# Kernel optimization log

Measured on AMD Instinct MI355X. Metric: run time of the kernel, lower is better.

## Reference

```python
import jax, jax.numpy as jnp
import numpy as np

HIDDEN_DIM = 512
SCALE = HIDDEN_DIM ** (-0.5)


def setup_inputs() -> dict:
    key = jax.random.key(0)
    kx, kw = jax.random.split(key)
    x = jax.random.normal(kx, (4, 4096, HIDDEN_DIM), dtype=jnp.float32)
    # nn.Linear weight is [out, in]; y = x @ W.T. We store W in torch layout.
    Wq = jax.random.normal(kw, (HIDDEN_DIM, HIDDEN_DIM), dtype=jnp.float32) * (HIDDEN_DIM ** -0.5)
    return {"x": x, "Wq": Wq}


def reference(x, Wq):
    # Faithful to source: q, k, v all use the SAME q_matrix projection.
    q = jnp.einsum("bcd,ed->bce", x, Wq)  # [B, C, D]
    k = q
    v = q
    scores = jnp.einsum("bcd,bed->bce", q, k) * SCALE  # [B, C, C]
    attn = jax.nn.softmax(scores, axis=-1)
    # dropout p=0.0 -> identity
    y = jnp.einsum("bce,bed->bcd", attn, v)  # [B, C, D]
    return y
```

## Files before the change

### kernel.cpp

```cpp
#include <hip/hip_runtime.h>
#include <stdint.h>

typedef unsigned int u32;
typedef unsigned short u16;
typedef __attribute__((ext_vector_type(8))) short bf16x8;
typedef __attribute__((ext_vector_type(4))) float f32x4;

#define B_ 4
#define S_ 4096
#define D_ 512
#define SCALE_ 0.04419417382415922f

__device__ __forceinline__ u16 f2b(float f) {
  u32 u = __builtin_bit_cast(u32, f);
  return (u16)((u + 0x7FFFu + ((u >> 16) & 1u)) >> 16);
}
__device__ __forceinline__ float b2f(u16 h) {
  u32 u = ((u32)h) << 16;
  return __builtin_bit_cast(float, u);
}
__device__ __forceinline__ void gld16(const void* g, void* l) {
  __builtin_amdgcn_global_load_lds(
      (const __attribute__((address_space(1))) u32*)g,
      (__attribute__((address_space(3))) u32*)l, 16, 0, 0);
}

__global__ __launch_bounds__(256, 1) void qproj(
    const float* __restrict__ X, const float* __restrict__ W,
    u16* __restrict__ Qr, u16* __restrict__ Qt) {
  __shared__ __align__(16) u16 Wt[512 * 64];
  const int tid = threadIdx.x;
  const int wave = tid >> 6, lane = tid & 63;
  const int m16 = lane & 15, quad = lane >> 4;
  const int r0 = blockIdx.x * 64;

  f32x4 acc[32];
#pragma unroll
  for (int i = 0; i < 32; ++i) acc[i] = f32x4{};

  const float* xrow = X + (size_t)(r0 + wave * 16 + m16) * D_;

  for (int kc = 0; kc < 8; ++kc) {
#pragma unroll
    for (int rr = 0; rr < 2; ++rr) {
      int e = tid + rr * 256;
      const float* src = W + (size_t)e * D_ + kc * 64;
#pragma unroll
      for (int bl = 0; bl < 8; ++bl) {
        float4 a = ((const float4*)src)[bl * 2];
        float4 b = ((const float4*)src)[bl * 2 + 1];
        bf16x8 v;
        v[0] = (short)f2b(a.x); v[1] = (short)f2b(a.y);
        v[2] = (short)f2b(a.z); v[3] = (short)f2b(a.w);
        v[4] = (short)f2b(b.x); v[5] = (short)f2b(b.y);
        v[6] = (short)f2b(b.z); v[7] = (short)f2b(b.w);
        *(bf16x8*)(&Wt[e * 64 + ((bl + e) & 7) * 8]) = v;
      }
    }
    __syncthreads();
#pragma unroll
    for (int kk = 0; kk < 2; ++kk) {
      const float* ap = xrow + kc * 64 + kk * 32 + quad * 8;
      float4 a0 = ((const float4*)ap)[0];
      float4 a1 = ((const float4*)ap)[1];
      bf16x8 af;
      af[0] = (short)f2b(a0.x); af[1] = (short)f2b(a0.y);
      af[2] = (short)f2b(a0.z); af[3] = (short)f2b(a0.w);
      af[4] = (short)f2b(a1.x); af[5] = (short)f2b(a1.y);
      af[6] = (short)f2b(a1.z); af[7] = (short)f2b(a1.w);
      int jb = quad + 4 * kk;
#pragma unroll
      for (int nt = 0; nt < 32; ++nt) {
        int e = m16 + nt * 16;
        bf16x8 bf = *(const bf16x8*)(&Wt[e * 64 + ((jb + e) & 7) * 8]);
        acc[nt] = __builtin_amdgcn_mfma_f32_16x16x32_bf16(af, bf, acc[nt], 0, 0, 0);
      }
    }
    __syncthreads();
  }
  const int b = r0 >> 12;
  const int s0 = (r0 & (S_ - 1)) + wave * 16 + quad * 4;
  const int grow = r0 + wave * 16 + quad * 4;
#pragma unroll
  for (int nt = 0; nt < 32; ++nt) {
    int e = nt * 16 + m16;
    u16 h0 = f2b(acc[nt][0]), h1 = f2b(acc[nt][1]);
    u16 h2 = f2b(acc[nt][2]), h3 = f2b(acc[nt][3]);
    Qr[(size_t)(grow + 0) * D_ + e] = h0;
    Qr[(size_t)(grow + 1) * D_ + e] = h1;
    Qr[(size_t)(grow + 2) * D_ + e] = h2;
    Qr[(size_t)(grow + 3) * D_ + e] = h3;
    uint2 pv;
    pv.x = (u32)h0 | ((u32)h1 << 16);
    pv.y = (u32)h2 | ((u32)h3 << 16);
    *(uint2*)(&Qt[((size_t)(b * D_ + e)) * S_ + s0]) = pv;
  }
}

__global__ __launch_bounds__(256, 1) void flashattn(
    const u16* __restrict__ Qrow, const u16* __restrict__ Qt,
    float* __restrict__ Out) {
  __shared__ __align__(16) u16 Kt[64 * 512];
  __shared__ __align__(16) u16 Vt[512 * 64];
  __shared__ __align__(16) u16 Pl[4][16 * 88];

  const int tid = threadIdx.x;
  const int wave = tid >> 6, lane = tid & 63;
  const int m16 = lane & 15, quad = lane >> 4;
  const int qt = blockIdx.x, bb = blockIdx.y;
  const u16* Qb  = Qrow + (size_t)bb * S_ * D_;
  const u16* Qtb = Qt   + (size_t)bb * D_ * S_;

  bf16x8 qf[16];
  {
    const u16* qp = Qb + (size_t)(qt * 64 + wave * 16 + m16) * D_ + quad * 8;
#pragma unroll
    for (int ks = 0; ks < 16; ++ks) qf[ks] = *(const bf16x8*)(qp + ks * 32);
  }

  f32x4 o[32];
#pragma unroll
  for (int i = 0; i < 32; ++i) o[i] = f32x4{};
  float mrow[4] = {-1e30f, -1e30f, -1e30f, -1e30f};
  float lrow[4] = {0.f, 0.f, 0.f, 0.f};
  u16* pw = &Pl[wave][0];

  for (int kt = 0; kt < 64; ++kt) {
    {
      const u16* src = Qb + (size_t)(kt * 64) * D_;
#pragma unroll
      for (int t = 0; t < 16; ++t) {
        int n = wave * 16 + t;
        int gb = (lane & ~7) | ((lane + n) & 7);
        gld16(src + (size_t)n * D_ + gb * 8, &Kt[n * 512]);
      }
      const u16* vsrc = Qtb + kt * 64;
#pragma unroll
      for (int t = 0; t < 16; ++t) {
        int d0 = (wave * 16 + t) * 8;
        int d  = d0 + (lane >> 3);
        int gb = ((lane & 7) + d) & 7;
        gld16(vsrc + (size_t)d * S_ + gb * 8, &Vt[d0 * 64]);
      }
    }
    __syncthreads();

    f32x4 sv[4];
#pragma unroll
    for (int nt = 0; nt < 4; ++nt) {
      f32x4 a = f32x4{};
      int n = m16 + nt * 16;
      const u16* kr = &Kt[n * 512];
#pragma unroll
      for (int ks = 0; ks < 16; ++ks) {
        int jb = quad + 4 * ks;
        int ib = (jb & ~7) | ((jb - n) & 7);
        bf16x8 bf = *(const bf16x8*)(kr + ib * 8);
        a = __builtin_amdgcn_mfma_f32_16x16x32_bf16(qf[ks], bf, a, 0, 0, 0);
      }
      sv[nt] = a;
    }

    float mnew[4], alpha[4];
    int grew = 0;
#pragma unroll
    for (int r = 0; r < 4; ++r) {
      float t = fmaxf(fmaxf(sv[0][r], sv[1][r]), fmaxf(sv[2][r], sv[3][r]));
      t = fmaxf(t, __shfl_xor(t, 1));
      t = fmaxf(t, __shfl_xor(t, 2));
      t = fmaxf(t, __shfl_xor(t, 4));
      t = fmaxf(t, __shfl_xor(t, 8));
      float mn = fmaxf(mrow[r], t);
      mnew[r] = mn;
      grew |= (mn > mrow[r]);
      alpha[r] = __expf((mrow[r] - mn) * SCALE_);
    }
    float psum[4] = {0.f, 0.f, 0.f, 0.f};
#pragma unroll
    for (int nt = 0; nt < 4; ++nt) {
#pragma unroll
      for (int r = 0; r < 4; ++r) {
        float p = __expf((sv[nt][r] - mnew[r]) * SCALE_);
        u16 h = f2b(p);
        psum[r] += b2f(h);
        pw[(quad * 4 + r) * 88 + nt * 16 + m16] = h;
      }
    }
#pragma unroll
    for (int r = 0; r < 4; ++r) {
      float t = psum[r];
      t += __shfl_xor(t, 1);
      t += __shfl_xor(t, 2);
      t += __shfl_xor(t, 4);
      t += __shfl_xor(t, 8);
      lrow[r] = lrow[r] * alpha[r] + t;
      mrow[r] = mnew[r];
    }
    if (__ballot(grew) != 0ull) {
#pragma unroll
      for (int dt = 0; dt < 32; ++dt) {
        o[dt][0] *= alpha[0]; o[dt][1] *= alpha[1];
        o[dt][2] *= alpha[2]; o[dt][3] *= alpha[3];
      }
    }

#pragma unroll
    for (int ks2 = 0; ks2 < 2; ++ks2) {
      bf16x8 pf = *(const bf16x8*)(pw + m16 * 88 + ks2 * 32 + quad * 8);
      int ib = ((quad + 4 * ks2) - m16) & 7;
#pragma unroll
      for (int dt = 0; dt < 32; ++dt) {
        int d = m16 + dt * 16;
        bf16x8 vf = *(const bf16x8*)(&Vt[d * 64 + ib * 8]);
        o[dt] = __builtin_amdgcn_mfma_f32_16x16x32_bf16(pf, vf, o[dt], 0, 0, 0);
      }
    }
    __syncthreads();
  }

  float inv[4];
#pragma unroll
  for (int r = 0; r < 4; ++r) inv[r] = 1.f / lrow[r];
  const int row0 = qt * 64 + wave * 16 + quad * 4;
#pragma unroll
  for (int dt = 0; dt < 32; ++dt) {
    int col = dt * 16 + m16;
    size_t base = ((size_t)bb * S_ + row0) * D_ + col;
    Out[base]           = o[dt][0] * inv[0];
    Out[base + D_]      = o[dt][1] * inv[1];
    Out[base + 2 * D_]  = o[dt][2] * inv[2];
    Out[base + 3 * D_]  = o[dt][3] * inv[3];
  }
}

extern "C" void kernel_launch(void* const* d_in, const int* in_sizes, int n_in,
                              void* d_out, int out_size, void* d_ws, size_t ws_size,
                              hipStream_t stream) {
  (void)in_sizes; (void)n_in; (void)out_size; (void)ws_size;
  const float* X = (const float*)d_in[0];
  const float* W = (const float*)d_in[1];
  float* Out = (float*)d_out;
  u16* Qr = (u16*)d_ws;
  u16* Qt = Qr + (size_t)B_ * S_ * D_;

  qproj<<<dim3(256), dim3(256), 0, stream>>>(X, W, Qr, Qt);
  flashattn<<<dim3(64, 4), dim3(256), 0, stream>>>(Qr, Qt, Out);
}
```

Measured before the change: 432.3 us.

## Pipeline K/V staging in attention, precast W, and compute row sums via MFMA

The attention loop now issues V loads at the start of each tile and prefetches the next K tile after the score phase, which overlaps global-to-LDS transfers with compute. The per-row softmax denominator is no longer built with shuffle reductions; an extra MFMA against a ones vector accumulates it instead. A new kernel converts W to bf16 once per call, and the projection kernel double-buffers W tiles through async LDS loads while holding X fragments in registers. P is rounded with a cheaper bf16 conversion. The costs are an extra kernel launch, more register pressure in qproj, and an added barrier per attention tile.

```diff
diff --git a/kernel.cpp b/kernel.cpp
--- a/kernel.cpp
+++ b/kernel.cpp
@@ -15,9 +15,9 @@
   u32 u = __builtin_bit_cast(u32, f);
   return (u16)((u + 0x7FFFu + ((u >> 16) & 1u)) >> 16);
 }
-__device__ __forceinline__ float b2f(u16 h) {
-  u32 u = ((u32)h) << 16;
-  return __builtin_bit_cast(float, u);
+__device__ __forceinline__ u16 f2b_fast(float f) {
+  u32 u = __builtin_bit_cast(u32, f);
+  return (u16)((u + 0x8000u) >> 16);
 }
 __device__ __forceinline__ void gld16(const void* g, void* l) {
   __builtin_amdgcn_global_load_lds(
@@ -25,59 +25,73 @@
       (__attribute__((address_space(3))) u32*)l, 16, 0, 0);
 }
 
+__global__ __launch_bounds__(256, 1) void qprep(
+    const float* __restrict__ W, u16* __restrict__ Wb) {
+  int i = (blockIdx.x * 256 + threadIdx.x) * 4;
+  float4 a = *(const float4*)(W + i);
+  ushort4 o;
+  o.x = f2b(a.x); o.y = f2b(a.y); o.z = f2b(a.z); o.w = f2b(a.w);
+  *(ushort4*)(Wb + i) = o;
+}
+
 __global__ __launch_bounds__(256, 1) void qproj(
-    const float* __restrict__ X, const float* __restrict__ W,
+    const float* __restrict__ X, const u16* __restrict__ Wb,
     u16* __restrict__ Qr, u16* __restrict__ Qt) {
-  __shared__ __align__(16) u16 Wt[512 * 64];
+  __shared__ __align__(16) u16 Wt[2][512 * 64];
   const int tid = threadIdx.x;
   const int wave = tid >> 6, lane = tid & 63;
   const int m16 = lane & 15, quad = lane >> 4;
   const int r0 = blockIdx.x * 64;
 
+  const float* xrow = X + (size_t)(r0 + wave * 16 + m16) * D_;
+  bf16x8 af[16];
+#pragma unroll
+  for (int ks = 0; ks < 16; ++ks) {
+    const float* ap = xrow + ks * 32 + quad * 8;
+    float4 a0 = ((const float4*)ap)[0];
+    float4 a1 = ((const float4*)ap)[1];
+    bf16x8 v;
+    v[0] = (short)f2b(a0.x); v[1] = (short)f2b(a0.y);
+    v[2] = (short)f2b(a0.z); v[3] = (short)f2b(a0.w);
+    v[4] = (short)f2b(a1.x); v[5] = (short)f2b(a1.y);
+    v[6] = (short)f2b(a1.z); v[7] = (short)f2b(a1.w);
+    af[ks] = v;
+  }
+
   f32x4 acc[32];
 #pragma unroll
   for (int i = 0; i < 32; ++i) acc[i] = f32x4{};
 
-  const float* xrow = X + (size_t)(r0 + wave * 16 + m16) * D_;
+  auto stage = [&](int kc, int buf) {
+#pragma unroll
+    for (int t = 0; t < 16; ++t) {
+      int e0 = (wave * 16 + t) * 8;
+      int e = e0 + (lane >> 3);
+      int gb = ((lane & 7) - e) & 7;
+      gld16(Wb + (size_t)e * D_ + kc * 64 + gb * 8, &Wt[buf][e0 * 64]);
+    }
+  };
+
+  stage(0, 0);
+  __syncthreads();
 
   for (int kc = 0; kc < 8; ++kc) {
-#pragma unroll
-    for (int rr = 0; rr < 2; ++rr) {
-      int e = tid + rr * 256;
-      const float* src = W + (size_t)e * D_ + kc * 64;
-#pragma unroll
-      for (int bl = 0; bl < 8; ++bl) {
-        float4 a = ((const float4*)src)[bl * 2];
-        float4 b = ((const float4*)src)[bl * 2 + 1];
-        bf16x8 v;
-        v[0] = (short)f2b(a.x); v[1] = (short)f2b(a.y);
-        v[2] = (short)f2b(a.z); v[3] = (short)f2b(a.w);
-        v[4] = (short)f2b(b.x); v[5] = (short)f2b(b.y);
-        v[6] = (short)f2b(b.z); v[7] = (short)f2b(b.w);
-        *(bf16x8*)(&Wt[e * 64 + ((bl + e) & 7) * 8]) = v;
-      }
-    }
-    __syncthreads();
+    if (kc < 7) stage(kc + 1, (kc + 1) & 1);
+    const u16* wb = &Wt[kc & 1][0];
 #pragma unroll
     for (int kk = 0; kk < 2; ++kk) {
-      const float* ap = xrow + kc * 64 + kk * 32 + quad * 8;
-      float4 a0 = ((const float4*)ap)[0];
-      float4 a1 = ((const float4*)ap)[1];
-      bf16x8 af;
-      af[0] = (short)f2b(a0.x); af[1] = (short)f2b(a0.y);
-      af[2] = (short)f2b(a0.z); af[3] = (short)f2b(a0.w);
-      af[4] = (short)f2b(a1.x); af[5] = (short)f2b(a1.y);
-      af[6] = (short)f2b(a1.z); af[7] = (short)f2b(a1.w);
       int jb = quad + 4 * kk;
+      bf16x8 a = af[kc * 2 + kk];
 #pragma unroll
       for (int nt = 0; nt < 32; ++nt) {
         int e = m16 + nt * 16;
-        bf16x8 bf = *(const bf16x8*)(&Wt[e * 64 + ((jb + e) & 7) * 8]);
-        acc[nt] = __builtin_amdgcn_mfma_f32_16x16x32_bf16(af, bf, acc[nt], 0, 0, 0);
+        bf16x8 bf = *(const bf16x8*)(wb + e * 64 + ((jb + e) & 7) * 8);
+        acc[nt] = __builtin_amdgcn_mfma_f32_16x16x32_bf16(a, bf, acc[nt], 0, 0, 0);
       }
     }
     __syncthreads();
   }
+
   const int b = r0 >> 12;
   const int s0 = (r0 & (S_ - 1)) + wave * 16 + quad * 4;
   const int grow = r0 + wave * 16 + quad * 4;
@@ -111,6 +125,26 @@
   const u16* Qb  = Qrow + (size_t)bb * S_ * D_;
   const u16* Qtb = Qt   + (size_t)bb * D_ * S_;
 
+  auto stageK = [&](int kt) {
+    const u16* src = Qb + (size_t)(kt * 64) * D_;
+#pragma unroll
+    for (int t = 0; t < 16; ++t) {
+      int n = wave * 16 + t;
+      int gb = (lane & ~7) | ((lane + n) & 7);
+      gld16(src + (size_t)n * D_ + gb * 8, &Kt[n * 512]);
+    }
+  };
+  auto stageV = [&](int kt) {
+    const u16* vsrc = Qtb + kt * 64;
+#pragma unroll
+    for (int t = 0; t < 16; ++t) {
+      int d0 = (wave * 16 + t) * 8;
+      int d  = d0 + (lane >> 3);
+      int gb = ((lane & 7) + d) & 7;
+      gld16(vsrc + (size_t)d * S_ + gb * 8, &Vt[d0 * 64]);
+    }
+  };
+
   bf16x8 qf[16];
   {
     const u16* qp = Qb + (size_t)(qt * 64 + wave * 16 + m16) * D_ + quad * 8;
@@ -118,32 +152,22 @@
     for (int ks = 0; ks < 16; ++ks) qf[ks] = *(const bf16x8*)(qp + ks * 32);
   }
 
+  bf16x8 onesf;
+#pragma unroll
+  for (int j = 0; j < 8; ++j) onesf[j] = (short)0x3F80;
+
   f32x4 o[32];
 #pragma unroll
   for (int i = 0; i < 32; ++i) o[i] = f32x4{};
+  f32x4 ol = f32x4{};
   float mrow[4] = {-1e30f, -1e30f, -1e30f, -1e30f};
-  float lrow[4] = {0.f, 0.f, 0.f, 0.f};
   u16* pw = &Pl[wave][0];
 
+  stageK(0);
+  __syncthreads();
+
   for (int kt = 0; kt < 64; ++kt) {
-    {
-      const u16* src = Qb + (size_t)(kt * 64) * D_;
-#pragma unroll
-      for (int t = 0; t < 16; ++t) {
-        int n = wave * 16 + t;
-        int gb = (lane & ~7) | ((lane + n) & 7);
-        gld16(src + (size_t)n * D_ + gb * 8, &Kt[n * 512]);
-      }
-      const u16* vsrc = Qtb + kt * 64;
-#pragma unroll
-      for (int t = 0; t < 16; ++t) {
-        int d0 = (wave * 16 + t) * 8;
-        int d  = d0 + (lane >> 3);
-        int gb = ((lane & 7) + d) & 7;
-        gld16(vsrc + (size_t)d * S_ + gb * 8, &Vt[d0 * 64]);
-      }
-    }
-    __syncthreads();
+    stageV(kt);
 
     f32x4 sv[4];
 #pragma unroll
@@ -174,34 +198,29 @@
       mnew[r] = mn;
       grew |= (mn > mrow[r]);
       alpha[r] = __expf((mrow[r] - mn) * SCALE_);
-    }
-    float psum[4] = {0.f, 0.f, 0.f, 0.f};
+      mrow[r] = mn;
+    }
 #pragma unroll
     for (int nt = 0; nt < 4; ++nt) {
 #pragma unroll
       for (int r = 0; r < 4; ++r) {
         float p = __expf((sv[nt][r] - mnew[r]) * SCALE_);
-        u16 h = f2b(p);
-        psum[r] += b2f(h);
-        pw[(quad * 4 + r) * 88 + nt * 16 + m16] = h;
-      }
-    }
-#pragma unroll
-    for (int r = 0; r < 4; ++r) {
-      float t = psum[r];
-      t += __shfl_xor(t, 1);
-      t += __shfl_xor(t, 2);
-      t += __shfl_xor(t, 4);
-      t += __shfl_xor(t, 8);
-      lrow[r] = lrow[r] * alpha[r] + t;
-      mrow[r] = mnew[r];
-    }
+        pw[(quad * 4 + r) * 88 + nt * 16 + m16] = f2b_fast(p);
+      }
+    }
+
+    __syncthreads();
+
+    if (kt < 63) stageK(kt + 1);
+
     if (__ballot(grew) != 0ull) {
 #pragma unroll
       for (int dt = 0; dt < 32; ++dt) {
         o[dt][0] *= alpha[0]; o[dt][1] *= alpha[1];
         o[dt][2] *= alpha[2]; o[dt][3] *= alpha[3];
       }
+      ol[0] *= alpha[0]; ol[1] *= alpha[1];
+      ol[2] *= alpha[2]; ol[3] *= alpha[3];
     }
 
 #pragma unroll
@@ -214,13 +233,15 @@
         bf16x8 vf = *(const bf16x8*)(&Vt[d * 64 + ib * 8]);
         o[dt] = __builtin_amdgcn_mfma_f32_16x16x32_bf16(pf, vf, o[dt], 0, 0, 0);
       }
-    }
+      ol = __builtin_amdgcn_mfma_f32_16x16x32_bf16(pf, onesf, ol, 0, 0, 0);
+    }
+
     __syncthreads();
   }
 
   float inv[4];
 #pragma unroll
-  for (int r = 0; r < 4; ++r) inv[r] = 1.f / lrow[r];
+  for (int r = 0; r < 4; ++r) inv[r] = 1.f / ol[r];
   const int row0 = qt * 64 + wave * 16 + quad * 4;
 #pragma unroll
   for (int dt = 0; dt < 32; ++dt) {
@@ -242,7 +263,9 @@
   float* Out = (float*)d_out;
   u16* Qr = (u16*)d_ws;
   u16* Qt = Qr + (size_t)B_ * S_ * D_;
-
-  qproj<<<dim3(256), dim3(256), 0, stream>>>(X, W, Qr, Qt);
+  u16* Wb = Qt + (size_t)B_ * D_ * S_;
+
+  qprep<<<dim3(256), dim3(256), 0, stream>>>(W, Wb);
+  qproj<<<dim3(256), dim3(256), 0, stream>>>(X, Wb, Qr, Qt);
   flashattn<<<dim3(64, 4), dim3(256), 0, stream>>>(Qr, Qt, Out);
 }
```

Result: faster. 356.0 us (-17.6%).
